# Performance work log

Measured on AMD Instinct MI355X. Metric: run time of the kernel, lower is better.

The kernel has to match this reference:

```python
import jax, jax.numpy as jnp
import numpy as np

B, L, D = 4, 2048, 1024
H, DK, DV = 4, 256, 256
CHUNK = 32
MIN_FLOOR, MAX_FLOOR = 0.01, 0.1
EPS = 1e-5


def _l2norm(x):
    return x * jax.lax.rsqrt(jnp.sum(x * x, -1, keepdims=True) + 1e-6)


def _causal_dwconv(x, w):
    # x: [b, L, C], w: [C, k] -> depthwise causal 1d conv
    b, l, c = x.shape
    k = w.shape[-1]
    xt = jnp.transpose(x, (0, 2, 1))
    y = jax.lax.conv_general_dilated(xt, w[:, None, :], (1,), [(k - 1, 0)],
                                     dimension_numbers=('NCH', 'OIH', 'NCH'),
                                     feature_group_count=c)
    return jnp.transpose(y, (0, 2, 1))


def _delta_rule_chunkwise(q, k, v, beta, chunk=CHUNK):
    # q,k: [b,h,L,dk]; v: [b,h,L,dv]; beta: [b,h,L]; L % chunk == 0
    b, h, l, dk = q.shape
    dv = v.shape[-1]
    q = _l2norm(q)
    k = _l2norm(k)
    v = v * beta[..., None]
    kb = k * beta[..., None]
    n = l // chunk
    resh = lambda t: t.reshape(b, h, n, chunk, t.shape[-1])
    q, k, v, kb = resh(q), resh(k), resh(v), resh(kb)
    tri = jnp.triu(jnp.ones((chunk, chunk), bool))        # incl diag
    strict = jnp.triu(jnp.ones((chunk, chunk), bool), 1)  # excl diag
    att = jnp.where(tri, 0.0, -(kb @ jnp.swapaxes(k, -1, -2)))
    # UT transform: forward substitution building (I - lower)^{-1}
    for i in range(1, chunk):
        upd = jnp.einsum('bhnj,bhnjk->bhnk', att[..., i, :], att)
        att = att.at[..., i, :i].add(upd[..., :i])
    att = att + jnp.eye(chunk, dtype=att.dtype)
    u = att @ v
    w = att @ kb

    def step(S, xs):
        q_i, k_i, u_i, w_i = xs  # [b,h,chunk,d]
        local = jnp.where(strict, 0.0, q_i @ jnp.swapaxes(k_i, -1, -2))
        u_adj = u_i - w_i @ S
        o_i = q_i @ S + local @ u_adj
        return S + jnp.swapaxes(k_i, -1, -2) @ u_adj, o_i

    xs = tuple(jnp.moveaxis(t, 2, 0) for t in (q, k, u, w))
    S0 = jnp.zeros((b, h, dk, dv), q.dtype)
    S, o = jax.lax.scan(step, S0, xs)
    return jnp.moveaxis(o, 0, 2).reshape(b, h, l, dv), S


def _rmsnorm(x, w):
    return x * jax.lax.rsqrt(jnp.mean(x * x, -1, keepdims=True) + EPS) * w


def setup_inputs():
    key = jax.random.key(0)
    ks = jax.random.split(key, 16)
    s = 0.02
    return {
        'hidden_states': jax.random.normal(ks[0], (B, L, D), jnp.float32),
        'W_q': jax.random.normal(ks[1], (D, H * DK), jnp.float32) * s,
        'W_k': jax.random.normal(ks[2], (D, H * DK), jnp.float32) * s,
        'W_v': jax.random.normal(ks[3], (D, H * DV), jnp.float32) * s,
        'W_b': jax.random.normal(ks[4], (D, H), jnp.float32) * s,
        'conv_w_q': jax.random.normal(ks[5], (H * DK, 4), jnp.float32) * 0.3,
        'conv_w_k': jax.random.normal(ks[6], (H * DK, 4), jnp.float32) * 0.3,
        'conv_w_v': jax.random.normal(ks[7], (H * DV, 4), jnp.float32) * 0.3,
        'fir_short_w': jax.random.normal(ks[8], (H, DV, 3), jnp.float32) * 0.1,
        'fir_long_w': jax.random.normal(ks[9], (H, DV, 31), jnp.float32) * 0.1,
        'W_fuse1': jax.random.normal(ks[10], (D + 3 * H * DV, 2 * D), jnp.float32) * s,
        'b_fuse1': jnp.zeros((2 * D,), jnp.float32),
        'W_fuse2': jax.random.normal(ks[11], (2 * D, H * 4), jnp.float32) * s,
        'b_fuse2': jnp.zeros((H * 4,), jnp.float32).at[3::4].set(4.0),
        'others_log_tau': jnp.zeros((H,), jnp.float32),
        'norm_w': jnp.ones((DV,), jnp.float32),
        'W_o': jax.random.normal(ks[12], (H * DV, D), jnp.float32) * s,
    }


def reference(hidden_states, W_q, W_k, W_v, W_b, conv_w_q, conv_w_k, conv_w_v,
              fir_short_w, fir_long_w, W_fuse1, b_fuse1, W_fuse2, b_fuse2,
              others_log_tau, norm_w, W_o):
    b, l, d = hidden_states.shape
    # projections + mandatory short conv (silu activation)
    q = jax.nn.silu(_causal_dwconv(hidden_states @ W_q, conv_w_q))
    k = jax.nn.silu(_causal_dwconv(hidden_states @ W_k, conv_w_k))
    v = jax.nn.silu(_causal_dwconv(hidden_states @ W_v, conv_w_v))
    q = q.reshape(b, l, H, DK)
    k = k.reshape(b, l, H, DK)
    v = v.reshape(b, l, H, DV)
    beta = jax.nn.sigmoid(hidden_states @ W_b)  # [b,l,H]
    delta_out, _ = _delta_rule_chunkwise(
        jnp.transpose(q, (0, 2, 1, 3)), jnp.transpose(k, (0, 2, 1, 3)),
        jnp.transpose(v, (0, 2, 1, 3)), jnp.transpose(beta, (0, 2, 1)))
    delta_out = jnp.transpose(delta_out, (0, 2, 1, 3))  # [b,l,H,DV]
    # depthwise FIR paths on v
    vc = v.reshape(b, l, H * DV)
    fir_s = _causal_dwconv(vc, fir_short_w.reshape(H * DV, -1)).reshape(b, l, H, DV)
    fir_l = _causal_dwconv(vc, fir_long_w.reshape(H * DV, -1)).reshape(b, l, H, DV)
    # fusion gate MLP
    gate_in = jnp.concatenate([hidden_states, fir_s.reshape(b, l, -1),
                               fir_l.reshape(b, l, -1), delta_out.reshape(b, l, -1)], -1)
    hid = jax.nn.gelu(gate_in @ W_fuse1 + b_fuse1, approximate=False)
    logits = (hid @ W_fuse2 + b_fuse2).reshape(b, l, H, 4)
    p_raw = jax.nn.sigmoid(logits[..., 3])
    # token-adaptive context floor
    floor = MIN_FLOOR + (MAX_FLOOR - MIN_FLOOR) * (1.0 - p_raw)
    p_val = (1.0 - floor) * p_raw
    tau = jnp.exp(others_log_tau)  # per-head temperature
    others = jax.nn.softmax(logits[..., :3] / tau[None, None, :, None], -1)
    p_ctx = (1.0 - p_val)[..., None] * others
    o = (p_ctx[..., 0:1] * fir_s + p_ctx[..., 1:2] * fir_l +
         p_ctx[..., 2:3] * delta_out + p_val[..., None] * v)
    o = _rmsnorm(o, norm_w)
    return o.reshape(b, l, H * DV) @ W_o
```

## Files before the change

### kernel.cpp

```cpp
#include <hip/hip_runtime.h>
#include <hip/hip_bf16.h>

#define B_ 4
#define L_ 2048
#define D_ 1024
#define H_ 4
#define DK_ 256
#define DV_ 256
#define NCH 64
#define NTOK 8192

typedef __attribute__((ext_vector_type(8))) short bf16x8;
typedef __attribute__((ext_vector_type(4))) float f32x4;
typedef unsigned int u32;

__device__ __forceinline__ float bu2f(unsigned short u) {
    union { unsigned int i; float f; } x; x.i = ((unsigned int)u) << 16; return x.f;
}
__device__ __forceinline__ unsigned short f2bu(float f) {
    union { __hip_bfloat16 h; unsigned short u; } x; x.h = __float2bfloat16(f); return x.u;
}
#define MFMA16(a, b, c) __builtin_amdgcn_mfma_f32_16x16x32_bf16(a, b, c, 0, 0, 0)

__device__ __forceinline__ void gload16(const void* g, void* l) {
    __builtin_amdgcn_global_load_lds(
        (const __attribute__((address_space(1))) u32*)g,
        (__attribute__((address_space(3))) u32*)l, 16, 0, 0);
}

__global__ __launch_bounds__(256) void k_transpose(const float* __restrict__ in,
                                                   unsigned short* __restrict__ out,
                                                   int K, int N) {
    __shared__ float tile[32][33];
    int k0 = blockIdx.y * 32, n0 = blockIdx.x * 32;
    int tx = threadIdx.x & 31, ty = threadIdx.x >> 5;
#pragma unroll
    for (int r = 0; r < 4; ++r)
        tile[ty + 8 * r][tx] = in[(long)(k0 + ty + 8 * r) * N + n0 + tx];
    __syncthreads();
#pragma unroll
    for (int r = 0; r < 4; ++r)
        out[(long)(n0 + ty + 8 * r) * K + k0 + tx] = f2bu(tile[tx][ty + 8 * r]);
}

__global__ __launch_bounds__(256) void k_padT2(const float* __restrict__ W,
                                               unsigned short* __restrict__ out) {
    long idx = (long)blockIdx.x * 256 + threadIdx.x;
    int n = (int)(idx >> 11), k = (int)(idx & 2047);
    out[idx] = (n < 16) ? f2bu(W[k * 16 + n]) : (unsigned short)0;
}

__global__ __launch_bounds__(256) void k_cvt_hs(const float4* __restrict__ hs4,
                                                unsigned short* __restrict__ gate_in) {
    int idx = blockIdx.x * 256 + threadIdx.x;
    float4 v = hs4[idx];
    int row = idx >> 8;
    int c4 = (idx & 255) * 4;
    ushort4 o;
    o.x = f2bu(v.x); o.y = f2bu(v.y); o.z = f2bu(v.z); o.w = f2bu(v.w);
    *reinterpret_cast<ushort4*>(&gate_in[(long)row * 4096 + c4]) = o;
}

__global__ __launch_bounds__(64) void k_beta(const float* __restrict__ hs,
                                             const float* __restrict__ W_b,
                                             float* __restrict__ beta) {
    int tok = blockIdx.x;
    int lane = threadIdx.x;
    const float* hrow = hs + (long)tok * D_;
    float acc0 = 0, acc1 = 0, acc2 = 0, acc3 = 0;
    for (int c = lane; c < D_; c += 64) {
        float x = hrow[c];
        float4 wb = reinterpret_cast<const float4*>(W_b)[c];
        acc0 += x * wb.x; acc1 += x * wb.y; acc2 += x * wb.z; acc3 += x * wb.w;
    }
#pragma unroll
    for (int off = 32; off; off >>= 1) {
        acc0 += __shfl_down(acc0, off);
        acc1 += __shfl_down(acc1, off);
        acc2 += __shfl_down(acc2, off);
        acc3 += __shfl_down(acc3, off);
    }
    if (lane == 0) {
        int b = tok >> 11, l = tok & 2047;
        beta[((long)(b * H_ + 0)) * L_ + l] = 1.f / (1.f + expf(-acc0));
        beta[((long)(b * H_ + 1)) * L_ + l] = 1.f / (1.f + expf(-acc1));
        beta[((long)(b * H_ + 2)) * L_ + l] = 1.f / (1.f + expf(-acc2));
        beta[((long)(b * H_ + 3)) * L_ + l] = 1.f / (1.f + expf(-acc3));
    }
}

template <int EPI>
__global__ __launch_bounds__(256) void k_gemm(const unsigned short* __restrict__ A, int lda,
                                              const unsigned short* __restrict__ BT, int ldb,
                                              void* __restrict__ Cout, int ldc,
                                              const float* __restrict__ bias,
                                              int K, int gx) {
    __shared__ __align__(16) unsigned short As[128][64];
    __shared__ __align__(16) unsigned short Bs[128][64];
    const int tid = threadIdx.x;
    const int wave = tid >> 6, lane = tid & 63;
    const int wm = wave & 1, wn = wave >> 1;
    const int lr = lane & 15, lg = lane >> 4;
    const int nwg = gridDim.x;
    const int cpx = nwg >> 3;
    const int orig = blockIdx.x;
    const int wg = (orig & 7) * cpx + (orig >> 3);
    const int m0 = (wg / gx) * 128, n0 = (wg % gx) * 128;
    const int srow = wave * 32 + (lane >> 3);
    const int scol = (((lane & 7) ^ ((lane >> 3) & 7))) * 8;
    const unsigned short* Ap = &A[(long)(m0 + srow) * lda + scol];
    const unsigned short* Bp = &BT[(long)(n0 + srow) * ldb + scol];
    unsigned short* AsB = &As[wave * 32][0];
    unsigned short* BsB = &Bs[wave * 32][0];
    const unsigned short* AsF = &As[0][0];
    const unsigned short* BsF = &Bs[0][0];
    f32x4 acc[4][4] = {};
    for (int k0 = 0; k0 < K; k0 += 64) {
#pragma unroll
        for (int g = 0; g < 4; ++g) {
            gload16(Ap + (long)g * 8 * lda + k0, AsB + g * 8 * 64);
            gload16(Bp + (long)g * 8 * ldb + k0, BsB + g * 8 * 64);
        }
        __syncthreads();
#pragma unroll
        for (int ks = 0; ks < 2; ++ks) {
            bf16x8 af[4], bfr[4];
#pragma unroll
            for (int mt = 0; mt < 4; ++mt) {
                int r = wm * 64 + mt * 16 + lr;
                af[mt] = *reinterpret_cast<const bf16x8*>(
                    AsF + r * 64 + (((ks * 4 + lg) ^ (lr & 7)) * 8));
            }
#pragma unroll
            for (int nt = 0; nt < 4; ++nt) {
                int r = wn * 64 + nt * 16 + lr;
                bfr[nt] = *reinterpret_cast<const bf16x8*>(
                    BsF + r * 64 + (((ks * 4 + lg) ^ (lr & 7)) * 8));
            }
#pragma unroll
            for (int mt = 0; mt < 4; ++mt)
#pragma unroll
                for (int nt = 0; nt < 4; ++nt)
                    acc[mt][nt] = MFMA16(af[mt], bfr[nt], acc[mt][nt]);
        }
        __syncthreads();
    }
#pragma unroll
    for (int mt = 0; mt < 4; ++mt)
#pragma unroll
        for (int nt = 0; nt < 4; ++nt)
#pragma unroll
            for (int r = 0; r < 4; ++r) {
                int row = m0 + wm * 64 + mt * 16 + lg * 4 + r;
                int col = n0 + wn * 64 + nt * 16 + lr;
                float v = acc[mt][nt][r];
                if (EPI == 2) {
                    v += bias[col];
                    v = 0.5f * v * (1.f + erff(v * 0.70710678118f));
                }
                if (EPI == 0)
                    reinterpret_cast<float*>(Cout)[(long)row * ldc + col] = v;
                else
                    reinterpret_cast<unsigned short*>(Cout)[(long)row * ldc + col] = f2bu(v);
            }
}

__global__ __launch_bounds__(256) void k_conv_silu(const unsigned short* __restrict__ QKVp,
                                                   const float* __restrict__ cwq,
                                                   const float* __restrict__ cwk,
                                                   const float* __restrict__ cwv,
                                                   unsigned short* __restrict__ qn,
                                                   unsigned short* __restrict__ kn,
                                                   unsigned short* __restrict__ v_blc) {
    int tok = blockIdx.x;
    int b = tok >> 11, l = tok & 2047;
    int t = threadIdx.x;
    float y[12];
#pragma unroll
    for (int j = 0; j < 12; ++j) {
        int c = t + 256 * j;
        const float* cw = (j < 4) ? &cwq[c * 4] : (j < 8) ? &cwk[(c - 1024) * 4] : &cwv[(c - 2048) * 4];
        float s = 0.f;
#pragma unroll
        for (int jj = 0; jj < 4; ++jj) {
            int tl = l - 3 + jj;
            if (tl >= 0) s += bu2f(QKVp[((long)(b * L_ + tl)) * 3072 + c]) * cw[jj];
        }
        y[j] = s / (1.f + expf(-s));
    }
    float sq[8];
#pragma unroll
    for (int j = 0; j < 8; ++j) sq[j] = y[j] * y[j];
    int wave = t >> 6, lane = t & 63;
#pragma unroll
    for (int off = 32; off; off >>= 1)
#pragma unroll
        for (int j = 0; j < 8; ++j) sq[j] += __shfl_down(sq[j], off);
    __shared__ float red[4][8];
    if (lane == 0)
#pragma unroll
        for (int j = 0; j < 8; ++j) red[wave][j] = sq[j];
    __syncthreads();
    float tot[8];
#pragma unroll
    for (int j = 0; j < 8; ++j) tot[j] = red[0][j] + red[1][j] + red[2][j] + red[3][j];
#pragma unroll
    for (int h = 0; h < 4; ++h) {
        float sc = rsqrtf(tot[h] + 1e-6f);
        qn[((long)(b * H_ + h) * L_ + l) * 256 + t] = f2bu(y[h] * sc);
    }
#pragma unroll
    for (int h = 0; h < 4; ++h) {
        float sc = rsqrtf(tot[4 + h] + 1e-6f);
        kn[((long)(b * H_ + h) * L_ + l) * 256 + t] = f2bu(y[4 + h] * sc);
    }
#pragma unroll
    for (int h = 0; h < 4; ++h)
        v_blc[(long)tok * 1024 + h * 256 + t] = f2bu(y[8 + h]);
}

__global__ __launch_bounds__(256) void k_delta_chunk(const unsigned short* __restrict__ qn,
                                                     const unsigned short* __restrict__ kn,
                                                     const unsigned short* __restrict__ v_blc,
                                                     const float* __restrict__ beta,
                                                     unsigned short* __restrict__ u_buf,
                                                     unsigned short* __restrict__ w_buf,
                                                     unsigned short* __restrict__ local_buf,
                                                     unsigned short* __restrict__ kT_buf) {
    int bid = blockIdx.x;
    int n = bid & 63, bh = bid >> 6;
    int b = bh >> 2, h = bh & 3;
    int t0 = n * 32;
    __shared__ __align__(16) unsigned short k_s[32][264];
    __shared__ __align__(16) unsigned short vbT[256][40];
    __shared__ __align__(16) unsigned short kbT[256][40];
    __shared__ __align__(16) float att[32][33];
    __shared__ __align__(16) unsigned short att_b[32][40];
    __shared__ float bet[32];
    int tid = threadIdx.x, wave = tid >> 6, lane = tid & 63;
    int lr = lane & 15, lg = lane >> 4;

    {
        int row = tid >> 3;
        int cc = (tid & 7) * 32;
        float brow = beta[(long)bh * L_ + t0 + row];
        if ((tid & 7) == 0) bet[row] = brow;
        const uint4* kp = reinterpret_cast<const uint4*>(&kn[((long)bh * L_ + t0 + row) * 256 + cc]);
        const uint4* vp = reinterpret_cast<const uint4*>(&v_blc[((long)(b * L_ + t0 + row)) * 1024 + h * 256 + cc]);
        unsigned short kv[32], vv[32];
#pragma unroll
        for (int g = 0; g < 4; ++g) {
            uint4 x = kp[g];
            *reinterpret_cast<uint4*>(&kv[g * 8]) = x;
            *reinterpret_cast<uint4*>(&k_s[row][cc + g * 8]) = x;
            *reinterpret_cast<uint4*>(&vv[g * 8]) = vp[g];
        }
#pragma unroll
        for (int e = 0; e < 32; ++e) {
            kbT[cc + e][row] = f2bu(bu2f(kv[e]) * brow);
            vbT[cc + e][row] = f2bu(bu2f(vv[e]) * brow);
        }
    }
    __syncthreads();

    {
        unsigned short tmp[32];
#pragma unroll
        for (int t = 0; t < 32; ++t) tmp[t] = k_s[t][tid];
#pragma unroll
        for (int g = 0; g < 4; ++g)
            *reinterpret_cast<uint4*>(&kT_buf[((long)bid * 256 + tid) * 32 + g * 8]) =
                *reinterpret_cast<uint4*>(&tmp[g * 8]);
    }

    {
        int i0 = (wave & 1) * 16, j0 = (wave >> 1) * 16;
        f32x4 G = {0, 0, 0, 0}, S2 = {0, 0, 0, 0};
#pragma unroll
        for (int kk = 0; kk < 8; ++kk) {
            bf16x8 bk = *reinterpret_cast<const bf16x8*>(&k_s[j0 + lr][kk * 32 + lg * 8]);
            bf16x8 ak = *reinterpret_cast<const bf16x8*>(&k_s[i0 + lr][kk * 32 + lg * 8]);
            bf16x8 aq = *reinterpret_cast<const bf16x8*>(&qn[((long)bh * L_ + t0 + i0 + lr) * 256 + kk * 32 + lg * 8]);
            G = MFMA16(ak, bk, G);
            S2 = MFMA16(aq, bk, S2);
        }
#pragma unroll
        for (int r = 0; r < 4; ++r) {
            int i = i0 + lg * 4 + r, j = j0 + lr;
            att[i][j] = (j < i) ? -bet[i] * G[r] : 0.f;
            local_buf[(long)bid * 1024 + i * 32 + j] = f2bu((j <= i) ? S2[r] : 0.f);
        }
    }
    __syncthreads();

    for (int i = 1; i < 32; ++i) {
        float upd = 0.f;
        if (tid < i) {
            for (int j = tid + 1; j < i; ++j) upd += att[i][j] * att[j][tid];
        }
        __syncthreads();
        if (tid < i) att[i][tid] += upd;
        __syncthreads();
    }
    for (int e = tid; e < 1024; e += 256) {
        int i = e >> 5, j = e & 31;
        att_b[i][j] = f2bu(att[i][j] + ((i == j) ? 1.f : 0.f));
    }
    __syncthreads();

    {
        int mt = wave & 1;
        bf16x8 afr = *reinterpret_cast<const bf16x8*>(&att_b[mt * 16 + lr][lg * 8]);
        f32x4 z = {0, 0, 0, 0};
#pragma unroll
        for (int ntt = 0; ntt < 8; ++ntt) {
            int n0c = (wave >> 1) * 128 + ntt * 16;
            bf16x8 bu = *reinterpret_cast<const bf16x8*>(&vbT[n0c + lr][lg * 8]);
            bf16x8 bw = *reinterpret_cast<const bf16x8*>(&kbT[n0c + lr][lg * 8]);
            f32x4 ut = MFMA16(afr, bu, z);
            f32x4 wt = MFMA16(afr, bw, z);
#pragma unroll
            for (int r = 0; r < 4; ++r) {
                int t = mt * 16 + lg * 4 + r, c = n0c + lr;
                u_buf[((long)bid * 32 + t) * 256 + c] = f2bu(ut[r]);
                w_buf[((long)bid * 32 + t) * 256 + c] = f2bu(wt[r]);
            }
        }
    }
}

__global__ __launch_bounds__(256) void k_scan(const unsigned short* __restrict__ qn,
                                              const unsigned short* __restrict__ u_buf,
                                              const unsigned short* __restrict__ w_buf,
                                              const unsigned short* __restrict__ local_buf,
                                              const unsigned short* __restrict__ kT_buf,
                                              unsigned short* __restrict__ gate_in) {
    int bid = blockIdx.x;
    int bh = bid & 15, dvb = bid >> 4;
    int b = bh >> 2, h = bh & 3;
    int dc0 = dvb * 16;
    __shared__ __align__(16) unsigned short Tb[16][264];
    __shared__ __align__(16) unsigned short uaT[16][40];
    const int tid = threadIdx.x, wave = tid >> 6, lane = tid & 63;
    const int lr = lane & 15, lg = lane >> 4;
    const int wi = wave & 1;
    const bool isW = wave < 2;
    const int c0w = wave * 64;
    f32x4 Tacc[4] = {};
    for (int e = tid; e < 16 * 264; e += 256) (&Tb[0][0])[e] = 0;
    const unsigned short* q_bh = qn + (long)bh * L_ * 256;
    const unsigned short* u_bh = u_buf + (long)bh * 64 * 8192;
    const unsigned short* w_bh = w_buf + (long)bh * 64 * 8192;
    const unsigned short* l_bh = local_buf + (long)bh * 64 * 1024;
    const unsigned short* kT_bh = kT_buf + (long)bh * 64 * 8192;
    const unsigned short* wq_base = (isW ? w_bh : q_bh) + (16 * wi + lr) * 256;
    const unsigned short* u_base = u_bh + (16 * wi + lg * 4) * 256 + dc0 + lr;
    const unsigned short* l_base = l_bh + (16 * wi + lr) * 32 + lg * 8;
    const unsigned short* kT_base = kT_bh + (c0w + lr) * 32 + lg * 8;
    bf16x8 wqA[8], kB[4], lA = {};
    float uv[4];
    auto prefetch = [&](int n) {
        long o8 = (long)n * 8192;
#pragma unroll
        for (int kk = 0; kk < 8; ++kk)
            wqA[kk] = *reinterpret_cast<const bf16x8*>(wq_base + o8 + kk * 32 + lg * 8);
#pragma unroll
        for (int cc = 0; cc < 4; ++cc)
            kB[cc] = *reinterpret_cast<const bf16x8*>(kT_base + o8 + cc * 512);
        if (isW) {
#pragma unroll
            for (int r = 0; r < 4; ++r) uv[r] = bu2f(u_base[o8 + r * 256]);
        } else {
            lA = *reinterpret_cast<const bf16x8*>(l_base + (long)n * 1024);
        }
    };
    prefetch(0);
    __syncthreads();
    for (int n = 0; n < 64; ++n) {
        f32x4 P0 = {0, 0, 0, 0}, P1 = {0, 0, 0, 0};
#pragma unroll
        for (int kk = 0; kk < 8; kk += 2) {
            bf16x8 t0 = *reinterpret_cast<const bf16x8*>(&Tb[lr][kk * 32 + lg * 8]);
            bf16x8 t1 = *reinterpret_cast<const bf16x8*>(&Tb[lr][(kk + 1) * 32 + lg * 8]);
            P0 = MFMA16(wqA[kk], t0, P0);
            P1 = MFMA16(wqA[kk + 1], t1, P1);
        }
        f32x4 P;
#pragma unroll
        for (int r = 0; r < 4; ++r) P[r] = P0[r] + P1[r];
        if (isW) {
#pragma unroll
            for (int r = 0; r < 4; ++r)
                uaT[lr][16 * wi + lg * 4 + r] = f2bu(uv[r] - P[r]);
        }
        bf16x8 kBc[4];
#pragma unroll
        for (int cc = 0; cc < 4; ++cc) kBc[cc] = kB[cc];
        bf16x8 lAc = lA;
        if (n + 1 < 64) prefetch(n + 1);
        __syncthreads();
        bf16x8 uaA = *reinterpret_cast<const bf16x8*>(&uaT[lr][lg * 8]);
        if (!isW) {
            f32x4 O = MFMA16(lAc, uaA, P);
#pragma unroll
            for (int r = 0; r < 4; ++r) {
                long row = (long)b * L_ + n * 32 + 16 * wi + lg * 4 + r;
                gate_in[row * 4096 + 3072 + h * 256 + dc0 + lr] = f2bu(O[r]);
            }
        }
#pragma unroll
        for (int cc = 0; cc < 4; ++cc)
            Tacc[cc] = MFMA16(uaA, kBc[cc], Tacc[cc]);
#pragma unroll
        for (int cc = 0; cc < 4; ++cc)
#pragma unroll
            for (int r = 0; r < 4; ++r)
                Tb[lg * 4 + r][c0w + cc * 16 + lr] = f2bu(Tacc[cc][r]);
        __syncthreads();
    }
}

__global__ __launch_bounds__(256) void k_fir(const unsigned short* __restrict__ v_blc,
                                             const float* __restrict__ ws3,
                                             const float* __restrict__ wl31,
                                             unsigned short* __restrict__ gate_in) {
    __shared__ unsigned short xs[94][256];
    int b = blockIdx.y, tt = blockIdx.x * 64, c0 = blockIdx.z * 256;
    int tid = threadIdx.x;
    for (int r = 0; r < 94; ++r) {
        int t = tt - 30 + r;
        xs[r][tid] = (t >= 0) ? v_blc[((long)(b * L_ + t)) * 1024 + c0 + tid] : (unsigned short)0;
    }
    int c = c0 + tid;
    float wl[31], ws[3];
#pragma unroll
    for (int j = 0; j < 31; ++j) wl[j] = wl31[(long)c * 31 + j];
#pragma unroll
    for (int j = 0; j < 3; ++j) ws[j] = ws3[(long)c * 3 + j];
    __syncthreads();
    for (int t = 0; t < 64; ++t) {
        float accl = 0.f, accs = 0.f;
#pragma unroll
        for (int j = 0; j < 31; ++j) accl += bu2f(xs[t + j][tid]) * wl[j];
#pragma unroll
        for (int j = 0; j < 3; ++j) accs += bu2f(xs[t + 28 + j][tid]) * ws[j];
        long row = (long)b * L_ + tt + t;
        gate_in[row * 4096 + 1024 + c] = f2bu(accs);
        gate_in[row * 4096 + 2048 + c] = f2bu(accl);
    }
}

__global__ __launch_bounds__(256) void k_gate(const float* __restrict__ logits_pre,
                                              const float* __restrict__ b_fuse2,
                                              const float* __restrict__ log_tau,
                                              const float* __restrict__ norm_w,
                                              const unsigned short* __restrict__ gate_in,
                                              const unsigned short* __restrict__ v_blc,
                                              unsigned short* __restrict__ o_norm) {
    int tok = blockIdx.x;
    int tid = threadIdx.x;
    __shared__ float lg_s[16];
    __shared__ float red[4][4];
    if (tid < 16) lg_s[tid] = logits_pre[(long)tok * 128 + tid] + b_fuse2[tid];
    __syncthreads();
    float o[4];
#pragma unroll
    for (int h = 0; h < 4; ++h) {
        float l0 = lg_s[h * 4 + 0], l1 = lg_s[h * 4 + 1], l2 = lg_s[h * 4 + 2], l3 = lg_s[h * 4 + 3];
        float praw = 1.f / (1.f + expf(-l3));
        float fl_ = 0.01f + 0.09f * (1.f - praw);
        float pval = (1.f - fl_) * praw;
        float itau = expf(-log_tau[h]);
        float a0 = l0 * itau, a1 = l1 * itau, a2 = l2 * itau;
        float m = fmaxf(a0, fmaxf(a1, a2));
        float e0 = expf(a0 - m), e1 = expf(a1 - m), e2 = expf(a2 - m);
        float inv = (1.f - pval) / (e0 + e1 + e2);
        long base = (long)tok * 4096;
        float fs = bu2f(gate_in[base + 1024 + h * 256 + tid]);
        float flv = bu2f(gate_in[base + 2048 + h * 256 + tid]);
        float dd = bu2f(gate_in[base + 3072 + h * 256 + tid]);
        float vv = bu2f(v_blc[(long)tok * 1024 + h * 256 + tid]);
        o[h] = e0 * inv * fs + e1 * inv * flv + e2 * inv * dd + pval * vv;
    }
    int wave = tid >> 6, lane = tid & 63;
    float s[4];
#pragma unroll
    for (int h = 0; h < 4; ++h) s[h] = o[h] * o[h];
#pragma unroll
    for (int off = 32; off; off >>= 1)
#pragma unroll
        for (int h = 0; h < 4; ++h) s[h] += __shfl_down(s[h], off);
    if (lane == 0)
#pragma unroll
        for (int h = 0; h < 4; ++h) red[wave][h] = s[h];
    __syncthreads();
#pragma unroll
    for (int h = 0; h < 4; ++h) {
        float tot = red[0][h] + red[1][h] + red[2][h] + red[3][h];
        float sc = rsqrtf(tot * (1.f / 256.f) + 1e-5f);
        o_norm[(long)tok * 1024 + h * 256 + tid] = f2bu(o[h] * sc * norm_w[tid]);
    }
}

extern "C" void kernel_launch(void* const* d_in, const int* in_sizes, int n_in,
                              void* d_out, int out_size, void* d_ws, size_t ws_size,
                              hipStream_t stream) {
    const float* hs = (const float*)d_in[0];
    const float* W_q = (const float*)d_in[1];
    const float* W_k = (const float*)d_in[2];
    const float* W_v = (const float*)d_in[3];
    const float* W_b = (const float*)d_in[4];
    const float* cwq = (const float*)d_in[5];
    const float* cwk = (const float*)d_in[6];
    const float* cwv = (const float*)d_in[7];
    const float* fir_s_w = (const float*)d_in[8];
    const float* fir_l_w = (const float*)d_in[9];
    const float* W_f1 = (const float*)d_in[10];
    const float* b_f1 = (const float*)d_in[11];
    const float* W_f2 = (const float*)d_in[12];
    const float* b_f2 = (const float*)d_in[13];
    const float* log_tau = (const float*)d_in[14];
    const float* norm_w = (const float*)d_in[15];
    const float* W_o = (const float*)d_in[16];

    char* ws = (char*)d_ws;
    size_t off = 0;
    auto alloc = [&](size_t bytes) { size_t o = off; off += (bytes + 255) & ~(size_t)255; return o; };
    unsigned short* gate_in = (unsigned short*)(ws + alloc((size_t)NTOK * 4096 * 2));
    unsigned short* QKVp    = (unsigned short*)(ws + alloc((size_t)NTOK * 3072 * 2));
    unsigned short* WqkvT   = (unsigned short*)(ws + alloc((size_t)3072 * 1024 * 2));
    unsigned short* Wf1T    = (unsigned short*)(ws + alloc((size_t)2048 * 4096 * 2));
    unsigned short* WoT     = (unsigned short*)(ws + alloc((size_t)1024 * 1024 * 2));
    unsigned short* Wf2Tp   = (unsigned short*)(ws + alloc((size_t)128 * 2048 * 2));
    float*          beta    = (float*)(ws + alloc((size_t)16 * 2048 * 4));
    unsigned short* qn      = (unsigned short*)(ws + alloc((size_t)16 * 2048 * 256 * 2));
    unsigned short* kn      = (unsigned short*)(ws + alloc((size_t)16 * 2048 * 256 * 2));
    unsigned short* v_blc   = (unsigned short*)(ws + alloc((size_t)NTOK * 1024 * 2));
    unsigned short* u_buf   = (unsigned short*)(ws + alloc((size_t)16 * 64 * 8192 * 2));
    unsigned short* w_buf   = (unsigned short*)(ws + alloc((size_t)16 * 64 * 8192 * 2));
    unsigned short* locb    = (unsigned short*)(ws + alloc((size_t)16 * 64 * 1024 * 2));
    unsigned short* kT_buf  = (unsigned short*)(ws + alloc((size_t)16 * 64 * 8192 * 2));
    float*          logits  = (float*)(ws + alloc((size_t)NTOK * 128 * 4));
    unsigned short* o_norm  = (unsigned short*)(ws + alloc((size_t)NTOK * 1024 * 2));
    unsigned short* hid     = QKVp;

    k_transpose<<<dim3(32, 32), 256, 0, stream>>>(W_q, WqkvT, 1024, 1024);
    k_transpose<<<dim3(32, 32), 256, 0, stream>>>(W_k, WqkvT + (size_t)1024 * 1024, 1024, 1024);
    k_transpose<<<dim3(32, 32), 256, 0, stream>>>(W_v, WqkvT + (size_t)2048 * 1024, 1024, 1024);
    k_transpose<<<dim3(64, 128), 256, 0, stream>>>(W_f1, Wf1T, 4096, 2048);
    k_transpose<<<dim3(32, 32), 256, 0, stream>>>(W_o, WoT, 1024, 1024);
    k_padT2<<<1024, 256, 0, stream>>>(W_f2, Wf2Tp);
    k_cvt_hs<<<8192, 256, 0, stream>>>((const float4*)hs, gate_in);
    k_beta<<<8192, 64, 0, stream>>>(hs, W_b, beta);
    k_gemm<1><<<24 * 64, 256, 0, stream>>>(gate_in, 4096, WqkvT, 1024, QKVp, 3072, nullptr,
                                           1024, 24);
    k_conv_silu<<<8192, 256, 0, stream>>>(QKVp, cwq, cwk, cwv, qn, kn, v_blc);
    k_delta_chunk<<<1024, 256, 0, stream>>>(qn, kn, v_blc, beta, u_buf, w_buf, locb, kT_buf);
    k_scan<<<256, 256, 0, stream>>>(qn, u_buf, w_buf, locb, kT_buf, gate_in);
    k_fir<<<dim3(32, 4, 4), 256, 0, stream>>>(v_blc, fir_s_w, fir_l_w, gate_in);
    k_gemm<2><<<16 * 64, 256, 0, stream>>>(gate_in, 4096, Wf1T, 4096, hid, 2048, b_f1,
                                           4096, 16);
    k_gemm<0><<<1 * 64, 256, 0, stream>>>(hid, 2048, Wf2Tp, 2048, logits, 128, nullptr,
                                          2048, 1);
    k_gate<<<8192, 256, 0, stream>>>(logits, b_f2, log_tau, norm_w, gate_in, v_blc, o_norm);
    k_gemm<0><<<8 * 64, 256, 0, stream>>>(o_norm, 1024, WoT, 1024, (float*)d_out, 1024, nullptr,
                                          1024, 8);
}
```

Measured before the change: 732.1 us.

## Fuse hs conversion with beta, split-K narrow fuse2 GEMM, add gemm occupancy hint

Merges the bf16 conversion of hidden_states and the beta projection into one kernel that reads each token row once. It also replaces the padded 128-wide GEMM for the 16-output fusion layer with a dedicated split-K MFMA kernel, which writes four partial logit buffers that k_gate sums. Finally it adds a min-blocks-per-CU hint of 3 to k_gemm, which may constrain registers and cause spills. The aim is to cut wasted work on the padded columns, expose more parallelism in the small GEMM, and save one kernel launch.

```diff
diff --git a/kernel.cpp b/kernel.cpp
--- a/kernel.cpp
+++ b/kernel.cpp
@@ -50,51 +50,48 @@
     out[idx] = (n < 16) ? f2bu(W[k * 16 + n]) : (unsigned short)0;
 }
 
-__global__ __launch_bounds__(256) void k_cvt_hs(const float4* __restrict__ hs4,
-                                                unsigned short* __restrict__ gate_in) {
-    int idx = blockIdx.x * 256 + threadIdx.x;
-    float4 v = hs4[idx];
-    int row = idx >> 8;
-    int c4 = (idx & 255) * 4;
+__global__ __launch_bounds__(256) void k_cvt_beta(const float4* __restrict__ hs4,
+                                                  const float* __restrict__ W_b,
+                                                  unsigned short* __restrict__ gate_in,
+                                                  float* __restrict__ beta) {
+    int tok = blockIdx.x;
+    int tid = threadIdx.x;
+    float4 v = hs4[(long)tok * 256 + tid];
     ushort4 o;
     o.x = f2bu(v.x); o.y = f2bu(v.y); o.z = f2bu(v.z); o.w = f2bu(v.w);
-    *reinterpret_cast<ushort4*>(&gate_in[(long)row * 4096 + c4]) = o;
-}
-
-__global__ __launch_bounds__(64) void k_beta(const float* __restrict__ hs,
-                                             const float* __restrict__ W_b,
-                                             float* __restrict__ beta) {
-    int tok = blockIdx.x;
-    int lane = threadIdx.x;
-    const float* hrow = hs + (long)tok * D_;
-    float acc0 = 0, acc1 = 0, acc2 = 0, acc3 = 0;
-    for (int c = lane; c < D_; c += 64) {
-        float x = hrow[c];
-        float4 wb = reinterpret_cast<const float4*>(W_b)[c];
-        acc0 += x * wb.x; acc1 += x * wb.y; acc2 += x * wb.z; acc3 += x * wb.w;
-    }
-#pragma unroll
-    for (int off = 32; off; off >>= 1) {
-        acc0 += __shfl_down(acc0, off);
-        acc1 += __shfl_down(acc1, off);
-        acc2 += __shfl_down(acc2, off);
-        acc3 += __shfl_down(acc3, off);
-    }
-    if (lane == 0) {
+    *reinterpret_cast<ushort4*>(&gate_in[(long)tok * 4096 + tid * 4]) = o;
+    const float4* wb = reinterpret_cast<const float4*>(W_b);
+    int c4 = tid * 4;
+    float4 w0 = wb[c4], w1 = wb[c4 + 1], w2 = wb[c4 + 2], w3 = wb[c4 + 3];
+    float s[4];
+    s[0] = v.x * w0.x + v.y * w1.x + v.z * w2.x + v.w * w3.x;
+    s[1] = v.x * w0.y + v.y * w1.y + v.z * w2.y + v.w * w3.y;
+    s[2] = v.x * w0.z + v.y * w1.z + v.z * w2.z + v.w * w3.z;
+    s[3] = v.x * w0.w + v.y * w1.w + v.z * w2.w + v.w * w3.w;
+    int wave = tid >> 6, lane = tid & 63;
+#pragma unroll
+    for (int off = 32; off; off >>= 1)
+#pragma unroll
+        for (int h = 0; h < 4; ++h) s[h] += __shfl_down(s[h], off);
+    __shared__ float red[4][4];
+    if (lane == 0)
+#pragma unroll
+        for (int h = 0; h < 4; ++h) red[wave][h] = s[h];
+    __syncthreads();
+    if (tid < 4) {
+        int h = tid;
+        float tot = red[0][h] + red[1][h] + red[2][h] + red[3][h];
         int b = tok >> 11, l = tok & 2047;
-        beta[((long)(b * H_ + 0)) * L_ + l] = 1.f / (1.f + expf(-acc0));
-        beta[((long)(b * H_ + 1)) * L_ + l] = 1.f / (1.f + expf(-acc1));
-        beta[((long)(b * H_ + 2)) * L_ + l] = 1.f / (1.f + expf(-acc2));
-        beta[((long)(b * H_ + 3)) * L_ + l] = 1.f / (1.f + expf(-acc3));
+        beta[((long)(b * H_ + h)) * L_ + l] = 1.f / (1.f + expf(-tot));
     }
 }
 
 template <int EPI>
-__global__ __launch_bounds__(256) void k_gemm(const unsigned short* __restrict__ A, int lda,
-                                              const unsigned short* __restrict__ BT, int ldb,
-                                              void* __restrict__ Cout, int ldc,
-                                              const float* __restrict__ bias,
-                                              int K, int gx) {
+__global__ __launch_bounds__(256, 3) void k_gemm(const unsigned short* __restrict__ A, int lda,
+                                                 const unsigned short* __restrict__ BT, int ldb,
+                                                 void* __restrict__ Cout, int ldc,
+                                                 const float* __restrict__ bias,
+                                                 int K, int gx) {
     __shared__ __align__(16) unsigned short As[128][64];
     __shared__ __align__(16) unsigned short Bs[128][64];
     const int tid = threadIdx.x;
@@ -163,6 +160,34 @@
                 else
                     reinterpret_cast<unsigned short*>(Cout)[(long)row * ldc + col] = f2bu(v);
             }
+}
+
+__global__ __launch_bounds__(256) void k_fuse2(const unsigned short* __restrict__ hid,
+                                               const unsigned short* __restrict__ Wf2Tp,
+                                               float* __restrict__ logits4) {
+    const int mt = blockIdx.x, kq = blockIdx.y;
+    const int tid = threadIdx.x, wave = tid >> 6, lane = tid & 63;
+    const int lr = lane & 15, lg = lane >> 4;
+    const int m0 = mt * 128 + wave * 32;
+    const int kb = kq * 512;
+    const unsigned short* a0p = hid + (long)(m0 + lr) * 2048 + kb + lg * 8;
+    const unsigned short* a1p = a0p + (long)16 * 2048;
+    const unsigned short* bp = Wf2Tp + (long)lr * 2048 + kb + lg * 8;
+    f32x4 acc0 = {0, 0, 0, 0}, acc1 = {0, 0, 0, 0};
+#pragma unroll 4
+    for (int kk = 0; kk < 16; ++kk) {
+        bf16x8 a0 = *reinterpret_cast<const bf16x8*>(a0p + kk * 32);
+        bf16x8 a1 = *reinterpret_cast<const bf16x8*>(a1p + kk * 32);
+        bf16x8 b = *reinterpret_cast<const bf16x8*>(bp + kk * 32);
+        acc0 = MFMA16(a0, b, acc0);
+        acc1 = MFMA16(a1, b, acc1);
+    }
+    float* out = logits4 + (long)kq * NTOK * 16;
+#pragma unroll
+    for (int r = 0; r < 4; ++r) {
+        out[(long)(m0 + lg * 4 + r) * 16 + lr] = acc0[r];
+        out[(long)(m0 + 16 + lg * 4 + r) * 16 + lr] = acc1[r];
+    }
 }
 
 __global__ __launch_bounds__(256) void k_conv_silu(const unsigned short* __restrict__ QKVp,
@@ -450,7 +475,7 @@
     }
 }
 
-__global__ __launch_bounds__(256) void k_gate(const float* __restrict__ logits_pre,
+__global__ __launch_bounds__(256) void k_gate(const float* __restrict__ logits4,
                                               const float* __restrict__ b_fuse2,
                                               const float* __restrict__ log_tau,
                                               const float* __restrict__ norm_w,
@@ -461,7 +486,12 @@
     int tid = threadIdx.x;
     __shared__ float lg_s[16];
     __shared__ float red[4][4];
-    if (tid < 16) lg_s[tid] = logits_pre[(long)tok * 128 + tid] + b_fuse2[tid];
+    if (tid < 16) {
+        long o = (long)tok * 16 + tid;
+        lg_s[tid] = logits4[o] + logits4[(long)NTOK * 16 + o] +
+                    logits4[(long)2 * NTOK * 16 + o] + logits4[(long)3 * NTOK * 16 + o] +
+                    b_fuse2[tid];
+    }
     __syncthreads();
     float o[4];
 #pragma unroll
@@ -540,7 +570,7 @@
     unsigned short* w_buf   = (unsigned short*)(ws + alloc((size_t)16 * 64 * 8192 * 2));
     unsigned short* locb    = (unsigned short*)(ws + alloc((size_t)16 * 64 * 1024 * 2));
     unsigned short* kT_buf  = (unsigned short*)(ws + alloc((size_t)16 * 64 * 8192 * 2));
-    float*          logits  = (float*)(ws + alloc((size_t)NTOK * 128 * 4));
+    float*          logits4 = (float*)(ws + alloc((size_t)4 * NTOK * 16 * 4));
     unsigned short* o_norm  = (unsigned short*)(ws + alloc((size_t)NTOK * 1024 * 2));
     unsigned short* hid     = QKVp;
 
@@ -550,8 +580,7 @@
     k_transpose<<<dim3(64, 128), 256, 0, stream>>>(W_f1, Wf1T, 4096, 2048);
     k_transpose<<<dim3(32, 32), 256, 0, stream>>>(W_o, WoT, 1024, 1024);
     k_padT2<<<1024, 256, 0, stream>>>(W_f2, Wf2Tp);
-    k_cvt_hs<<<8192, 256, 0, stream>>>((const float4*)hs, gate_in);
-    k_beta<<<8192, 64, 0, stream>>>(hs, W_b, beta);
+    k_cvt_beta<<<8192, 256, 0, stream>>>((const float4*)hs, W_b, gate_in, beta);
     k_gemm<1><<<24 * 64, 256, 0, stream>>>(gate_in, 4096, WqkvT, 1024, QKVp, 3072, nullptr,
                                            1024, 24);
     k_conv_silu<<<8192, 256, 0, stream>>>(QKVp, cwq, cwk, cwv, qn, kn, v_blc);
@@ -560,9 +589,8 @@
     k_fir<<<dim3(32, 4, 4), 256, 0, stream>>>(v_blc, fir_s_w, fir_l_w, gate_in);
     k_gemm<2><<<16 * 64, 256, 0, stream>>>(gate_in, 4096, Wf1T, 4096, hid, 2048, b_f1,
                                            4096, 16);
-    k_gemm<0><<<1 * 64, 256, 0, stream>>>(hid, 2048, Wf2Tp, 2048, logits, 128, nullptr,
-                                          2048, 1);
-    k_gate<<<8192, 256, 0, stream>>>(logits, b_f2, log_tau, norm_w, gate_in, v_blc, o_norm);
+    k_fuse2<<<dim3(64, 4), 256, 0, stream>>>(hid, Wf2Tp, logits4);
+    k_gate<<<8192, 256, 0, stream>>>(logits4, b_f2, log_tau, norm_w, gate_in, v_blc, o_norm);
     k_gemm<0><<<8 * 64, 256, 0, stream>>>(o_norm, 1024, WoT, 1024, (float*)d_out, 1024, nullptr,
                                           1024, 8);
 }
```

Result: faster. 658.8 us (-10.0%).
